# Kernel tuning notes

Hardware: AMD Instinct MI355X
Metric: run time of the kernel (lower is better)

Reference implementation:

```python
import jax, jax.numpy as jnp
import numpy as np

# Configuration mirroring init_kwargs
B, H, W = 64, 40, 40          # batch, grid (image 1280 / stride 32)
A, C = 5, 80                  # anchors per cell, classes
MAX_BOXES = 100               # max_detection_boxes
SCORE_THR = 0.001             # nms_score_threshold
IOU_THR = 0.5                 # nms_iou_threshold


def setup_inputs() -> dict:
    key = jax.random.key(0)
    k1, k2 = jax.random.split(key)
    predictions = jax.random.normal(k1, (B, H, W, A * (5 + C)), dtype=jnp.float32)
    # anchor (w, h) in grid-cell units, positive
    anchors = jax.random.uniform(k2, (A, 2), dtype=jnp.float32, minval=0.5, maxval=8.0)
    return {"predictions": predictions, "anchors": anchors}


def decode_yolo(predictions, anchors):
    """YOLOv2-style decode -> normalized corner boxes and per-class scores."""
    b, h, w, _ = predictions.shape
    p = predictions.reshape(b, h, w, A, 5 + C)
    gy, gx = jnp.meshgrid(jnp.arange(h, dtype=jnp.float32),
                          jnp.arange(w, dtype=jnp.float32), indexing="ij")
    grid = jnp.stack([gx, gy], axis=-1)[None, :, :, None, :]   # [1,h,w,1,2]
    dims = jnp.array([w, h], dtype=jnp.float32)
    xy = (jax.nn.sigmoid(p[..., 0:2]) + grid) / dims           # normalized centers
    wh = jnp.exp(p[..., 2:4]) * anchors / dims                 # normalized sizes
    conf = jax.nn.sigmoid(p[..., 4:5])
    probs = jax.nn.softmax(p[..., 5:], axis=-1)
    scores = conf * probs                                      # [b,h,w,A,C]
    boxes = jnp.concatenate([xy - wh * 0.5, xy + wh * 0.5], axis=-1)  # x1,y1,x2,y2
    return boxes.reshape(b, -1, 4), scores.reshape(b, -1, C)


def nms_single(boxes, scores_all):
    """Greedy per-class NMS for one image. boxes [N,4], scores_all [N,C]."""
    cls_scores = jnp.max(scores_all, axis=-1)
    classes = jnp.argmax(scores_all, axis=-1)
    s0 = jnp.where(cls_scores > SCORE_THR, cls_scores, -1.0)
    area = jnp.maximum(boxes[:, 2] - boxes[:, 0], 0.0) * \
           jnp.maximum(boxes[:, 3] - boxes[:, 1], 0.0)

    def step(s, _):
        idx = jnp.argmax(s)
        sc = s[idx]
        box = boxes[idx]
        x1 = jnp.maximum(box[0], boxes[:, 0]); y1 = jnp.maximum(box[1], boxes[:, 1])
        x2 = jnp.minimum(box[2], boxes[:, 2]); y2 = jnp.minimum(box[3], boxes[:, 3])
        inter = jnp.maximum(x2 - x1, 0.0) * jnp.maximum(y2 - y1, 0.0)
        box_area = jnp.maximum(box[2] - box[0], 0.0) * jnp.maximum(box[3] - box[1], 0.0)
        iou = inter / (area + box_area - inter + 1e-8)
        suppress = (iou > IOU_THR) & (classes == classes[idx])
        s_new = jnp.where(suppress, -1.0, s).at[idx].set(-1.0)
        valid = sc > 0.0
        out_box = jnp.where(valid, box, 0.0)
        out_sc = jnp.where(valid, sc, 0.0)
        out_cl = jnp.where(valid, classes[idx], -1)
        return s_new, (out_box, out_sc, out_cl)

    _, (ob, osc, ocl) = jax.lax.scan(step, s0, None, length=MAX_BOXES)
    return ob, osc, ocl  # [MAX_BOXES,4], [MAX_BOXES], [MAX_BOXES]


def reference(predictions, anchors):
    boxes, scores = decode_yolo(predictions, anchors)
    sel_boxes, sel_scores, sel_classes = jax.vmap(nms_single)(boxes, scores)
    return sel_boxes, sel_scores, sel_classes
```

## Files before the change

### kernel.cpp

```cpp
#include <hip/hip_runtime.h>
#include <math.h>

#define B 64
#define H 40
#define W 40
#define A 5
#define C 80
#define NBOX (H*W*A)
#define FEAT (5+C)
#define MAXB 100
#define SCORE_THR 0.001f
#define IOU_THR 0.5f

#define DEC_BOXES 64
#define DEC_THREADS 64
#define DEC_LDS4 1408

#define HBINS 10240
#define BINBASE 119808
#define TARGET 512

#define BK 48
#define RCAP 1024

typedef unsigned long long u64;
typedef unsigned int u32;

__global__ __launch_bounds__(DEC_THREADS) void decode_kernel(
    const float* __restrict__ pred, const float* __restrict__ anchors,
    float* __restrict__ boxes_ws, float* __restrict__ s_ws, int* __restrict__ cls_ws)
{
    __shared__ float lds[DEC_LDS4 * 4];
    const int tid = threadIdx.x;
    const int base_box = blockIdx.x * DEC_BOXES;

    {
        const float4* src4 = (const float4*)pred;
        const long long base4 = (long long)base_box * FEAT / 4;
        const long long TOT4  = (long long)B * NBOX * FEAT / 4;
        #pragma unroll
        for (int i = 0; i < 22; ++i) {
            long long g4 = base4 + i*64 + tid;
            if (g4 >= TOT4) g4 = TOT4 - 1;
            __builtin_amdgcn_global_load_lds(
                (const __attribute__((address_space(1))) void*)(src4 + g4),
                (__attribute__((address_space(3))) void*)((char*)lds + i*1024),
                16, 0, 0);
        }
    }
    __syncthreads();

    const int box = base_box + tid;
    const float* l = lds + tid * FEAT;

    int img  = box / NBOX;
    int n    = box - img * NBOX;
    int cell = n / A;
    int a    = n - cell * A;
    int gx   = cell % W;
    int gy   = cell / W;

    float tx = l[0], ty = l[1], tw = l[2], th = l[3], tc = l[4];

    float lg[C];
    #pragma unroll
    for (int i = 0; i < C; ++i) lg[i] = l[5+i];

    float sx = 1.f / (1.f + expf(-tx));
    float sy = 1.f / (1.f + expf(-ty));
    float cx = (sx + (float)gx) / (float)W;
    float cy = (sy + (float)gy) / (float)H;
    float aw = anchors[a*2+0], ah = anchors[a*2+1];
    float bw = expf(tw) * aw / (float)W;
    float bh = expf(th) * ah / (float)H;
    float conf = 1.f / (1.f + expf(-tc));

    float mm[8];
    #pragma unroll
    for (int w = 0; w < 8; ++w) mm[w] = lg[w];
    #pragma unroll
    for (int i = 8; i < C; ++i) mm[i & 7] = fmaxf(mm[i & 7], lg[i]);
    float m = fmaxf(fmaxf(fmaxf(mm[0],mm[1]),fmaxf(mm[2],mm[3])),
                    fmaxf(fmaxf(mm[4],mm[5]),fmaxf(mm[6],mm[7])));

    float sum = 0.f;
    float bv[4] = {-1.f,-1.f,-1.f,-1.f};
    int   bi[4] = {0,0,0,0};
    #pragma unroll
    for (int i = 0; i < C; ++i) {
        float e = expf(lg[i] - m);
        sum += e;
        int w = i & 3;
        if (e > bv[w]) { bv[w] = e; bi[w] = i; }
    }
    float best_e = bv[0]; int best_c = bi[0];
    #pragma unroll
    for (int w = 1; w < 4; ++w) {
        if (bv[w] > best_e || (bv[w] == best_e && bi[w] < best_c)) { best_e = bv[w]; best_c = bi[w]; }
    }

    float score = conf * (best_e / sum);
    float s0 = (score > SCORE_THR) ? score : -1.0f;

    float x1 = cx - bw*0.5f, y1 = cy - bh*0.5f;
    float x2 = cx + bw*0.5f, y2 = cy + bh*0.5f;

    ((float4*)boxes_ws)[box] = make_float4(x1, y1, x2, y2);
    s_ws[box] = s0;
    cls_ws[box] = best_c;
}

__device__ __forceinline__ u64 wave_max_u64(u64 v) {
    #define STAGE(CTRL, RMASK) { \
        u32 lo = (u32)v, hi = (u32)(v >> 32); \
        u32 tlo = (u32)__builtin_amdgcn_update_dpp(0, (int)lo, CTRL, RMASK, 0xf, true); \
        u32 thi = (u32)__builtin_amdgcn_update_dpp(0, (int)hi, CTRL, RMASK, 0xf, true); \
        u64 t = ((u64)thi << 32) | (u64)tlo; \
        if (t > v) v = t; \
    }
    STAGE(0x111, 0xf)
    STAGE(0x112, 0xf)
    STAGE(0x114, 0xf)
    STAGE(0x118, 0xf)
    STAGE(0x142, 0xa)
    STAGE(0x143, 0xc)
    #undef STAGE
    u32 flo = (u32)__builtin_amdgcn_readlane((int)(u32)v, 63);
    u32 fhi = (u32)__builtin_amdgcn_readlane((int)(v >> 32), 63);
    return ((u64)fhi << 32) | (u64)flo;
}

__global__ __launch_bounds__(1024) void selnmsrank_kernel(
    const float* __restrict__ boxes_ws, const float* __restrict__ s_ws,
    const int* __restrict__ cls_ws, float* __restrict__ out)
{
    __shared__ __align__(16) char smem[HBINS * 4];
    int* hist  = (int*)smem;
    u64* bkey  = (u64*)smem;
    u64* ckeys = (u64*)(smem + 30720);
    int* bcnt  = (int*)(smem + 38912);
    __shared__ int wavesum[16];
    __shared__ int tbin_s;
    __shared__ int cnt;

    const int img  = blockIdx.x;
    const int tid  = threadIdx.x;
    const int lane = tid & 63;
    const int wid  = tid >> 6;
    const long long ib = (long long)img * NBOX;

    #pragma unroll
    for (int q = 0; q < HBINS/1024; ++q) hist[tid + q*1024] = 0;
    if (tid == 0) { tbin_s = 0; cnt = 0; }
    __syncthreads();

    float sc_r[8];
    #pragma unroll
    for (int k = 0; k < 8; ++k) {
        int j = tid + k*1024;
        float s = (j < NBOX) ? s_ws[ib + j] : -1.f;
        sc_r[k] = s;
        if (s > 0.f) {
            int b = (int)(__float_as_uint(s) >> 13) - BINBASE;
            b = max(0, min(HBINS-1, b));
            atomicAdd(&hist[b], 1);
        }
    }
    __syncthreads();

    int sum_r = 0;
    {
        int base = HBINS - 10*(tid+1);
        #pragma unroll
        for (int q = 0; q < 10; ++q) sum_r += hist[base + q];
    }
    int incl = sum_r;
    #pragma unroll
    for (int off = 1; off < 64; off <<= 1) {
        int o = __shfl_up(incl, off);
        if (lane >= off) incl += o;
    }
    if (lane == 63) wavesum[wid] = incl;
    __syncthreads();
    {
        int wbase = 0;
        for (int w = 0; w < wid; ++w) wbase += wavesum[w];
        int excl = wbase + incl - sum_r;
        if (excl < TARGET && excl + sum_r >= TARGET) {
            int cum = excl;
            for (int q = 0; q < 10; ++q) {
                int b = HBINS - 10*tid - 1 - q;
                cum += hist[b];
                if (cum >= TARGET) { tbin_s = b; break; }
            }
        }
    }
    __syncthreads();
    const int tb = tbin_s;

    if (tid < C) bcnt[tid] = 0;
    __syncthreads();

    #pragma unroll
    for (int k = 0; k < 8; ++k) {
        int j = tid + k*1024;
        float s = sc_r[k];
        if (j < NBOX && s > 0.f) {
            int b = (int)(__float_as_uint(s) >> 13) - BINBASE;
            b = max(0, min(HBINS-1, b));
            if (b >= tb) {
                int c = cls_ws[ib + j];
                int pos = atomicAdd(&bcnt[c], 1);
                if (pos < BK) {
                    u64 key = ((u64)__float_as_uint(s) << 32)
                            | ((u64)(NBOX - j) << 19)
                            | ((u64)pos << 13) | (u64)c;
                    bkey[c*BK + pos] = key;
                }
            }
        }
    }
    __syncthreads();

    for (int q = 0; q < 5; ++q) {
        const int c  = wid*5 + q;
        const int nb = min(bcnt[c], BK);

        u64 key = 0, keep = 0;
        float x1=0.f, y1=0.f, x2=0.f, y2=0.f, ar=0.f;
        if (lane < nb) {
            key = bkey[c*BK + lane];
            int bidx = NBOX - (int)((key >> 19) & 0x1FFF);
            float4 b4 = ((const float4*)boxes_ws)[ib + bidx];
            x1=b4.x; y1=b4.y; x2=b4.z; y2=b4.w;
            ar = fmaxf(x2-x1,0.f)*fmaxf(y2-y1,0.f);
        }

        for (int t = 0; t < BK; ++t) {
            u64 bk = wave_max_u64(key);
            if (bk == 0) break;
            int sl = (int)((bk >> 13) & 63);
            float sx1 = __shfl(x1, sl), sy1 = __shfl(y1, sl);
            float sx2 = __shfl(x2, sl), sy2 = __shfl(y2, sl);
            float sarea = fmaxf(sx2-sx1,0.f)*fmaxf(sy2-sy1,0.f);

            if (lane == sl) {
                keep = key;
                key = 0;
            } else if (key != 0) {
                float ix1 = fmaxf(sx1, x1);
                float iy1 = fmaxf(sy1, y1);
                float ix2 = fminf(sx2, x2);
                float iy2 = fminf(sy2, y2);
                float inter = fmaxf(ix2-ix1,0.f)*fmaxf(iy2-iy1,0.f);
                float iou = inter / (ar + sarea - inter + 1e-8f);
                if (iou > IOU_THR) key = 0;
            }
        }

        if (lane < BK) bkey[c*BK + lane] = keep;
    }
    __syncthreads();

    for (int i = tid; i < C*BK; i += 1024) {
        u64 k = bkey[i];
        if (k != 0) {
            int p = atomicAdd(&cnt, 1);
            if (p < RCAP) ckeys[p] = k;
        }
    }
    __syncthreads();
    const int m = min(cnt, RCAP);

    float* out_boxes  = out;
    float* out_scores = out + B*MAXB*4;
    float* out_cls    = out + B*MAXB*5;

    for (int i = tid; i < m; i += 1024) {
        u64 mine = ckeys[i];
        int r = 0;
        for (int j = 0; j < m; ++j) r += (ckeys[j] > mine) ? 1 : 0;
        if (r < MAXB) {
            int c    = (int)(mine & 127);
            int bidx = NBOX - (int)((mine >> 19) & 0x1FFF);
            float4 b4 = ((const float4*)boxes_ws)[ib + bidx];
            int o = img*MAXB + r;
            out_boxes[o*4+0] = b4.x; out_boxes[o*4+1] = b4.y;
            out_boxes[o*4+2] = b4.z; out_boxes[o*4+3] = b4.w;
            out_scores[o] = __uint_as_float((u32)(mine >> 32));
            out_cls[o]    = (float)c;
        }
    }

    int base = min(m, MAXB);
    for (int r = base + tid; r < MAXB; r += 1024) {
        int o = img*MAXB + r;
        out_boxes[o*4+0]=0.f; out_boxes[o*4+1]=0.f;
        out_boxes[o*4+2]=0.f; out_boxes[o*4+3]=0.f;
        out_scores[o]=0.f;
        out_cls[o]=-1.f;
    }
}

extern "C" void kernel_launch(void* const* d_in, const int* in_sizes, int n_in,
                              void* d_out, int out_size, void* d_ws, size_t ws_size,
                              hipStream_t stream) {
    const float* pred    = (const float*)d_in[0];
    const float* anchors = (const float*)d_in[1];
    float* out = (float*)d_out;

    char* p = (char*)d_ws;
    float*  boxes_ws  = (float*)p;              p += (size_t)B*NBOX*4*sizeof(float);
    float*  s_ws      = (float*)p;              p += (size_t)B*NBOX*sizeof(float);
    int*    cls_ws    = (int*)p;

    decode_kernel<<<(B*NBOX)/DEC_BOXES, DEC_THREADS, 0, stream>>>(
        pred, anchors, boxes_ws, s_ws, cls_ws);
    selnmsrank_kernel<<<B, 1024, 0, stream>>>(
        boxes_ws, s_ws, cls_ws, out);
}
```

Baseline: 283.6 us.

## Make decode kernel persistent with double-buffered LDS prefetch of prediction tiles

The decode kernel becomes a persistent grid of 768 single-wave blocks. Each block loops over 64-box tiles with a stride of the grid size. While the current tile is being computed, the next tile is loaded asynchronously into a second LDS buffer, with the aim of overlapping global-to-LDS loads with the softmax and box math. In exchange, LDS use per block doubles and far fewer waves are resident per CU, which may reduce how much memory traffic can be in flight. The barrier at the end of each iteration may also force the prefetch to finish early.

New measurement: 291.1 us. +2.7%, slower.

```diff
diff --git a/kernel.cpp b/kernel.cpp
--- a/kernel.cpp
+++ b/kernel.cpp
@@ -14,7 +14,10 @@
 
 #define DEC_BOXES 64
 #define DEC_THREADS 64
-#define DEC_LDS4 1408
+#define TILE_B4 1360
+#define BUFB 22528
+#define NT ((B*NBOX)/DEC_BOXES)
+#define GRIDN 768
 
 #define HBINS 10240
 #define BINBASE 119808
@@ -30,84 +33,96 @@
     const float* __restrict__ pred, const float* __restrict__ anchors,
     float* __restrict__ boxes_ws, float* __restrict__ s_ws, int* __restrict__ cls_ws)
 {
-    __shared__ float lds[DEC_LDS4 * 4];
+    __shared__ float lds[2 * BUFB / 4];
     const int tid = threadIdx.x;
-    const int base_box = blockIdx.x * DEC_BOXES;
-
-    {
-        const float4* src4 = (const float4*)pred;
-        const long long base4 = (long long)base_box * FEAT / 4;
-        const long long TOT4  = (long long)B * NBOX * FEAT / 4;
+    const long long TOT4 = (long long)NT * TILE_B4;
+
+    const float4* src4 = (const float4*)pred;
+    auto stage = [&](int t, int h) {
+        const long long base4 = (long long)t * TILE_B4;
         #pragma unroll
         for (int i = 0; i < 22; ++i) {
             long long g4 = base4 + i*64 + tid;
             if (g4 >= TOT4) g4 = TOT4 - 1;
             __builtin_amdgcn_global_load_lds(
                 (const __attribute__((address_space(1))) void*)(src4 + g4),
-                (__attribute__((address_space(3))) void*)((char*)lds + i*1024),
+                (__attribute__((address_space(3))) void*)((char*)lds + h*BUFB + i*1024),
                 16, 0, 0);
         }
-    }
-    __syncthreads();
-
-    const int box = base_box + tid;
-    const float* l = lds + tid * FEAT;
-
-    int img  = box / NBOX;
-    int n    = box - img * NBOX;
-    int cell = n / A;
-    int a    = n - cell * A;
-    int gx   = cell % W;
-    int gy   = cell / W;
-
-    float tx = l[0], ty = l[1], tw = l[2], th = l[3], tc = l[4];
-
-    float lg[C];
-    #pragma unroll
-    for (int i = 0; i < C; ++i) lg[i] = l[5+i];
-
-    float sx = 1.f / (1.f + expf(-tx));
-    float sy = 1.f / (1.f + expf(-ty));
-    float cx = (sx + (float)gx) / (float)W;
-    float cy = (sy + (float)gy) / (float)H;
-    float aw = anchors[a*2+0], ah = anchors[a*2+1];
-    float bw = expf(tw) * aw / (float)W;
-    float bh = expf(th) * ah / (float)H;
-    float conf = 1.f / (1.f + expf(-tc));
-
-    float mm[8];
-    #pragma unroll
-    for (int w = 0; w < 8; ++w) mm[w] = lg[w];
-    #pragma unroll
-    for (int i = 8; i < C; ++i) mm[i & 7] = fmaxf(mm[i & 7], lg[i]);
-    float m = fmaxf(fmaxf(fmaxf(mm[0],mm[1]),fmaxf(mm[2],mm[3])),
-                    fmaxf(fmaxf(mm[4],mm[5]),fmaxf(mm[6],mm[7])));
-
-    float sum = 0.f;
-    float bv[4] = {-1.f,-1.f,-1.f,-1.f};
-    int   bi[4] = {0,0,0,0};
-    #pragma unroll
-    for (int i = 0; i < C; ++i) {
-        float e = expf(lg[i] - m);
-        sum += e;
-        int w = i & 3;
-        if (e > bv[w]) { bv[w] = e; bi[w] = i; }
-    }
-    float best_e = bv[0]; int best_c = bi[0];
-    #pragma unroll
-    for (int w = 1; w < 4; ++w) {
-        if (bv[w] > best_e || (bv[w] == best_e && bi[w] < best_c)) { best_e = bv[w]; best_c = bi[w]; }
-    }
-
-    float score = conf * (best_e / sum);
-    float s0 = (score > SCORE_THR) ? score : -1.0f;
-
-    float x1 = cx - bw*0.5f, y1 = cy - bh*0.5f;
-    float x2 = cx + bw*0.5f, y2 = cy + bh*0.5f;
-
-    ((float4*)boxes_ws)[box] = make_float4(x1, y1, x2, y2);
-    s_ws[box] = s0;
-    cls_ws[box] = best_c;
+    };
+
+    int cur = 0;
+    int t = blockIdx.x;
+    if (t < NT) stage(t, 0);
+    __syncthreads();
+
+    while (t < NT) {
+        const int tn = t + GRIDN;
+        if (tn < NT) stage(tn, cur ^ 1);
+
+        const float* l = lds + (cur * (BUFB/4)) + tid * FEAT;
+        const int box = t * DEC_BOXES + tid;
+
+        int img  = box / NBOX;
+        int n    = box - img * NBOX;
+        int cell = n / A;
+        int a    = n - cell * A;
+        int gx   = cell % W;
+        int gy   = cell / W;
+
+        float tx = l[0], ty = l[1], tw = l[2], th = l[3], tc = l[4];
+
+        float lg[C];
+        #pragma unroll
+        for (int i = 0; i < C; ++i) lg[i] = l[5+i];
+
+        float sx = 1.f / (1.f + expf(-tx));
+        float sy = 1.f / (1.f + expf(-ty));
+        float cx = (sx + (float)gx) / (float)W;
+        float cy = (sy + (float)gy) / (float)H;
+        float aw = anchors[a*2+0], ah = anchors[a*2+1];
+        float bw = expf(tw) * aw / (float)W;
+        float bh = expf(th) * ah / (float)H;
+        float conf = 1.f / (1.f + expf(-tc));
+
+        float mm[8];
+        #pragma unroll
+        for (int w = 0; w < 8; ++w) mm[w] = lg[w];
+        #pragma unroll
+        for (int i = 8; i < C; ++i) mm[i & 7] = fmaxf(mm[i & 7], lg[i]);
+        float m = fmaxf(fmaxf(fmaxf(mm[0],mm[1]),fmaxf(mm[2],mm[3])),
+                        fmaxf(fmaxf(mm[4],mm[5]),fmaxf(mm[6],mm[7])));
+
+        float sum = 0.f;
+        float bv[4] = {-1.f,-1.f,-1.f,-1.f};
+        int   bi[4] = {0,0,0,0};
+        #pragma unroll
+        for (int i = 0; i < C; ++i) {
+            float e = expf(lg[i] - m);
+            sum += e;
+            int w = i & 3;
+            if (e > bv[w]) { bv[w] = e; bi[w] = i; }
+        }
+        float best_e = bv[0]; int best_c = bi[0];
+        #pragma unroll
+        for (int w = 1; w < 4; ++w) {
+            if (bv[w] > best_e || (bv[w] == best_e && bi[w] < best_c)) { best_e = bv[w]; best_c = bi[w]; }
+        }
+
+        float score = conf * (best_e / sum);
+        float s0 = (score > SCORE_THR) ? score : -1.0f;
+
+        float x1 = cx - bw*0.5f, y1 = cy - bh*0.5f;
+        float x2 = cx + bw*0.5f, y2 = cy + bh*0.5f;
+
+        ((float4*)boxes_ws)[box] = make_float4(x1, y1, x2, y2);
+        s_ws[box] = s0;
+        cls_ws[box] = best_c;
+
+        __syncthreads();
+        cur ^= 1;
+        t = tn;
+    }
 }
 
 __device__ __forceinline__ u64 wave_max_u64(u64 v) {
@@ -314,7 +329,7 @@
     float*  s_ws      = (float*)p;              p += (size_t)B*NBOX*sizeof(float);
     int*    cls_ws    = (int*)p;
 
-    decode_kernel<<<(B*NBOX)/DEC_BOXES, DEC_THREADS, 0, stream>>>(
+    decode_kernel<<<GRIDN, DEC_THREADS, 0, stream>>>(
         pred, anchors, boxes_ws, s_ws, cls_ws);
     selnmsrank_kernel<<<B, 1024, 0, stream>>>(
         boxes_ws, s_ws, cls_ws, out);
```
